# Kernel optimization log

Measured on AMD Instinct MI355X. Metric: run time of the kernel, lower is better.

The kernel has to match this reference:

```python
import jax, jax.numpy as jnp
import numpy as np

BETA = 10.0
EXTREMA = 10.0
LIK_BOUND = 1e-9
FILTERS = (1, 3, 3, 3, 3, 1)


def _sos_tanh(xf, sos_w, sos_b):
    # xf: (C,1,L). Sum-of-tanh staircase quantizer (StanH):
    # y = -extrema + sum_i 0.5*w_i*(tanh(beta*(x-b_i))+1)
    t = jnp.tanh(BETA * (xf[..., None] - sos_b))  # (C,1,L,NS)
    return -EXTREMA + jnp.sum(0.5 * sos_w * (t + 1.0), axis=-1)


def _logits_cumulative(v, mats, biases, factors):
    # v: (C,1,L); per-channel MLP with softplus-reparameterized matrices
    logits = v
    for i, m in enumerate(mats):
        logits = jnp.einsum('coi,cil->col', jax.nn.softplus(m), logits) + biases[i]
        if i < len(factors):
            logits = logits + jnp.tanh(factors[i]) * jnp.tanh(logits)
    return logits


def setup_inputs() -> dict:
    key = jax.random.key(0)
    ks = jax.random.split(key, 8)
    N, C, H, W = 8, 192, 32, 32
    NS = 60
    x = jax.random.normal(ks[0], (N, C, H, W), jnp.float32) * 3.0
    # positive step weights summing roughly to the full range
    sos_w = jax.random.uniform(ks[1], (NS,), jnp.float32, 0.1, 1.0)
    sos_w = sos_w / jnp.sum(sos_w) * (2.0 * EXTREMA)
    sos_b = jnp.linspace(-EXTREMA, EXTREMA, NS).astype(jnp.float32)
    scale = 10.0 ** (1.0 / 5.0)
    out = {'x': x, 'sos_w': sos_w, 'sos_b': sos_b}
    kk = jax.random.split(ks[2], 10)
    for i in range(5):
        init = float(np.log(np.expm1(1.0 / scale / FILTERS[i + 1])))
        out[f'm{i}'] = jnp.full((C, FILTERS[i + 1], FILTERS[i]), init, jnp.float32)
        out[f'c{i}'] = jax.random.uniform(kk[i], (C, FILTERS[i + 1], 1), jnp.float32, -0.5, 0.5)
        if i < 4:
            out[f'f{i}'] = jnp.zeros((C, FILTERS[i + 1], 1), jnp.float32)
    return out


def reference(x, sos_w, sos_b, m0, m1, m2, m3, m4, c0, c1, c2, c3, c4, f0, f1, f2, f3):
    N, C, H, W = x.shape
    mats = (m0, m1, m2, m3, m4)
    biases = (c0, c1, c2, c3, c4)
    factors = (f0, f1, f2, f3)
    # permute (N,C,H,W) -> (C,1,N*H*W) as in quantize()
    xf = jnp.transpose(x, (1, 0, 2, 3)).reshape(C, 1, -1)
    yq = _sos_tanh(xf, sos_w, sos_b)  # training-mode SoS quantization
    lower = _logits_cumulative(yq - 0.5, mats, biases, factors)
    upper = _logits_cumulative(yq + 0.5, mats, biases, factors)
    sign = jax.lax.stop_gradient(-jnp.sign(lower + upper))
    lik = jnp.abs(jax.nn.sigmoid(sign * upper) - jax.nn.sigmoid(sign * lower))
    lik = jnp.maximum(lik, LIK_BOUND)
    y_hat = jnp.transpose(yq.reshape(C, N, H, W), (1, 0, 2, 3))
    lik = jnp.transpose(lik.reshape(C, N, H, W), (1, 0, 2, 3))
    return y_hat, lik
```

## Files before the change

kernel.cpp:

```cpp
#include <hip/hip_runtime.h>
#include <math.h>

#define C_CH    192
#define HW_     1024
#define NPLANE  1536
#define TOTAL_  1572864
#define PPB     2
#define NBLK    (NPLANE / PPB)

#define LOG2E   1.4426950408889634f
#define KSOS    28.853900817779268f
#define INV_D   2.95f

#define LUT_L   512
#define LUT_X0  (-10.72f)
#define LUT_SPAN 21.44f
#define LUT_H   (LUT_SPAN / (LUT_L - 1))
#define LUT_IH  ((LUT_L - 1) / LUT_SPAN)

__device__ __forceinline__ float rcp_f(float v)  { return __builtin_amdgcn_rcpf(v); }
__device__ __forceinline__ float exp2_f(float v) { return __builtin_amdgcn_exp2f(v); }

__device__ __forceinline__ float fast_tanh(float z) {
  float e = exp2_f(z * (2.0f * LOG2E));
  return 1.0f - 2.0f * rcp_f(e + 1.0f);
}
__device__ __forceinline__ float fast_sigmoid(float z) {
  return rcp_f(1.0f + exp2_f(-z * LOG2E));
}
__device__ __forceinline__ float softplus_f(float v) {
  return log1pf(expf(v));
}

__device__ __forceinline__ float mlp_full(float v, const float* P) {
  float t, a0, a1, a2, d0, d1, d2;
  t = fmaf(P[27], v, P[33]); a0 = fmaf(P[46], fast_tanh(t), t);
  t = fmaf(P[28], v, P[34]); a1 = fmaf(P[47], fast_tanh(t), t);
  t = fmaf(P[29], v, P[35]); a2 = fmaf(P[48], fast_tanh(t), t);

  t = fmaf(P[2], a2, fmaf(P[1], a1, fmaf(P[0], a0, P[36]))); d0 = fmaf(P[49], fast_tanh(t), t);
  t = fmaf(P[5], a2, fmaf(P[4], a1, fmaf(P[3], a0, P[37]))); d1 = fmaf(P[50], fast_tanh(t), t);
  t = fmaf(P[8], a2, fmaf(P[7], a1, fmaf(P[6], a0, P[38]))); d2 = fmaf(P[51], fast_tanh(t), t);

  t = fmaf(P[11], d2, fmaf(P[10], d1, fmaf(P[9],  d0, P[39]))); a0 = fmaf(P[52], fast_tanh(t), t);
  t = fmaf(P[14], d2, fmaf(P[13], d1, fmaf(P[12], d0, P[40]))); a1 = fmaf(P[53], fast_tanh(t), t);
  t = fmaf(P[17], d2, fmaf(P[16], d1, fmaf(P[15], d0, P[41]))); a2 = fmaf(P[54], fast_tanh(t), t);

  t = fmaf(P[20], a2, fmaf(P[19], a1, fmaf(P[18], a0, P[42]))); d0 = fmaf(P[55], fast_tanh(t), t);
  t = fmaf(P[23], a2, fmaf(P[22], a1, fmaf(P[21], a0, P[43]))); d1 = fmaf(P[56], fast_tanh(t), t);
  t = fmaf(P[26], a2, fmaf(P[25], a1, fmaf(P[24], a0, P[44]))); d2 = fmaf(P[57], fast_tanh(t), t);

  return fmaf(P[32], d2, fmaf(P[31], d1, fmaf(P[30], d0, P[45])));
}

__device__ __forceinline__ float mlp_fast(float v, const float* P) {
  float a0, a1, a2, d0, d1, d2;
  a0 = fmaf(P[27], v, P[33]);
  a1 = fmaf(P[28], v, P[34]);
  a2 = fmaf(P[29], v, P[35]);

  d0 = fmaf(P[2], a2, fmaf(P[1], a1, fmaf(P[0], a0, P[36])));
  d1 = fmaf(P[5], a2, fmaf(P[4], a1, fmaf(P[3], a0, P[37])));
  d2 = fmaf(P[8], a2, fmaf(P[7], a1, fmaf(P[6], a0, P[38])));

  a0 = fmaf(P[11], d2, fmaf(P[10], d1, fmaf(P[9],  d0, P[39])));
  a1 = fmaf(P[14], d2, fmaf(P[13], d1, fmaf(P[12], d0, P[40])));
  a2 = fmaf(P[17], d2, fmaf(P[16], d1, fmaf(P[15], d0, P[41])));

  d0 = fmaf(P[20], a2, fmaf(P[19], a1, fmaf(P[18], a0, P[42])));
  d1 = fmaf(P[23], a2, fmaf(P[22], a1, fmaf(P[21], a0, P[43])));
  d2 = fmaf(P[26], a2, fmaf(P[25], a1, fmaf(P[24], a0, P[44])));

  return fmaf(P[32], d2, fmaf(P[31], d1, fmaf(P[30], d0, P[45])));
}

__device__ __forceinline__ void load_tables(
    int t, int c,
    const float* __restrict__ sos_w, const float* __restrict__ sos_b,
    const float* __restrict__ m0, const float* __restrict__ m1,
    const float* __restrict__ m2, const float* __restrict__ m3,
    const float* __restrict__ m4,
    const float* __restrict__ c0, const float* __restrict__ c1,
    const float* __restrict__ c2, const float* __restrict__ c3,
    const float* __restrict__ c4,
    const float* __restrict__ f0, const float* __restrict__ f1,
    const float* __restrict__ f2, const float* __restrict__ f3,
    float* s_w, float* s_kb, float* s_pw, float* s_p)
{
  if (t < 68) {
    float w = (t < 60) ? sos_w[t] : 0.0f;
    float b = (t < 60) ? sos_b[t] : 0.0f;
    s_w[t]  = w;
    s_kb[t] = KSOS * b;
  }
  if (t >= 64 && t < 128) {
    int i = t - 64;
    float v = (i < 60) ? sos_w[i] : 0.0f;
    float s = v;
    #pragma unroll
    for (int off = 1; off < 64; off <<= 1) {
      float o = __shfl_up(s, off, 64);
      if (i >= off) s += o;
    }
    if (i <= 60) s_pw[i] = s - v;
  }
  {
    int p = t - 128;
    if (p >= 0 && p < 58) {
      float val;
      if      (p <  9) val = softplus_f(m1[c*9 +  p      ]);
      else if (p < 18) val = softplus_f(m2[c*9 + (p -  9)]);
      else if (p < 27) val = softplus_f(m3[c*9 + (p - 18)]);
      else if (p < 30) val = softplus_f(m0[c*3 + (p - 27)]);
      else if (p < 33) val = softplus_f(m4[c*3 + (p - 30)]);
      else if (p < 36) val = c0[c*3 + (p - 33)];
      else if (p < 39) val = c1[c*3 + (p - 36)];
      else if (p < 42) val = c2[c*3 + (p - 39)];
      else if (p < 45) val = c3[c*3 + (p - 42)];
      else if (p < 46) val = c4[c];
      else if (p < 49) val = tanhf(f0[c*3 + (p - 46)]);
      else if (p < 52) val = tanhf(f1[c*3 + (p - 49)]);
      else if (p < 55) val = tanhf(f2[c*3 + (p - 52)]);
      else             val = tanhf(f3[c*3 + (p - 55)]);
      s_p[p] = val;
    }
  }
  __syncthreads();
}

__device__ __forceinline__ float sos_eval(
    float xx, const float* s_w, const float* s_kb, const float* s_pw)
{
  float kf = ceilf((xx + 9.32f) * INV_D);
  int k = (int)kf;
  k = max(0, min(60, k));
  float acc = s_pw[k];
  float kx  = KSOS * xx;
  #pragma unroll
  for (int i = 0; i < 6; ++i) {
    float z = s_kb[k + i] - kx;
    acc = fmaf(s_w[k + i], rcp_f(1.0f + exp2_f(z)), acc);
  }
  return acc - 10.0f;
}

template <bool FAST>
__device__ __forceinline__ float lik_from_y(float yq, const float* P) {
  float lo = FAST ? mlp_fast(yq - 0.5f, P) : mlp_full(yq - 0.5f, P);
  float up = FAST ? mlp_fast(yq + 0.5f, P) : mlp_full(yq + 0.5f, P);
  float lu = lo + up;
  float sg = (lu > 0.0f) ? -1.0f : ((lu < 0.0f) ? 1.0f : 0.0f);
  float lik = fabsf(fast_sigmoid(sg * up) - fast_sigmoid(sg * lo));
  return fmaxf(lik, 1e-9f);
}

__global__ __launch_bounds__(256)
void eb_fused(const float* __restrict__ x,
              const float* __restrict__ sos_w, const float* __restrict__ sos_b,
              const float* __restrict__ m0, const float* __restrict__ m1,
              const float* __restrict__ m2, const float* __restrict__ m3,
              const float* __restrict__ m4,
              const float* __restrict__ c0, const float* __restrict__ c1,
              const float* __restrict__ c2, const float* __restrict__ c3,
              const float* __restrict__ c4,
              const float* __restrict__ f0, const float* __restrict__ f1,
              const float* __restrict__ f2, const float* __restrict__ f3,
              float* __restrict__ out)
{
  __shared__ float s_w[68], s_kb[68], s_pw[64], s_p[58];
  __shared__ float s_y[LUT_L], s_l[LUT_L];

  const int t  = threadIdx.x;
  const int c  = blockIdx.x % C_CH;
  const int g  = blockIdx.x / C_CH;
  const int p0 = (2 * g)     * C_CH + c;
  const int p1 = (2 * g + 1) * C_CH + c;

  const int base0 = p0 * HW_;
  const int base1 = p1 * HW_;
  float4 xv0 = reinterpret_cast<const float4*>(x + base0)[t];
  float4 xv1 = reinterpret_cast<const float4*>(x + base1)[t];

  load_tables(t, c, sos_w, sos_b, m0, m1, m2, m3, m4,
              c0, c1, c2, c3, c4, f0, f1, f2, f3, s_w, s_kb, s_pw, s_p);

  float P[58];
  #pragma unroll
  for (int i = 0; i < 58; ++i) P[i] = s_p[i];

  bool nofac = true;
  #pragma unroll
  for (int i = 46; i < 58; ++i) nofac &= (P[i] == 0.0f);

  if (nofac) {
    #pragma unroll
    for (int r = 0; r < LUT_L / 256; ++r) {
      int idx = t + 256 * r;
      float xg = LUT_X0 + (float)idx * LUT_H;
      float yq = sos_eval(xg, s_w, s_kb, s_pw);
      s_y[idx] = yq;
      s_l[idx] = lik_from_y<true>(yq, P);
    }
  } else {
    #pragma unroll
    for (int r = 0; r < LUT_L / 256; ++r) {
      int idx = t + 256 * r;
      float xg = LUT_X0 + (float)idx * LUT_H;
      float yq = sos_eval(xg, s_w, s_kb, s_pw);
      s_y[idx] = yq;
      s_l[idx] = lik_from_y<false>(yq, P);
    }
  }
  __syncthreads();

  float4 xvs[PPB] = {xv0, xv1};
  int bases[PPB]  = {base0, base1};
  #pragma unroll
  for (int pl = 0; pl < PPB; ++pl) {
    float xs[4] = {xvs[pl].x, xvs[pl].y, xvs[pl].z, xvs[pl].w};
    float ys[4], ls[4];
    #pragma unroll
    for (int e = 0; e < 4; ++e) {
      float xx = fminf(fmaxf(xs[e], LUT_X0), LUT_X0 + LUT_SPAN);
      float u  = (xx - LUT_X0) * LUT_IH;
      int   i  = (int)u;
      i = min(i, LUT_L - 2);
      float fr = u - (float)i;
      float y0 = s_y[i], y1 = s_y[i + 1];
      float l0 = s_l[i], l1 = s_l[i + 1];
      ys[e] = fmaf(fr, y1 - y0, y0);
      ls[e] = fmaf(fr, l1 - l0, l0);
    }
    reinterpret_cast<float4*>(out + bases[pl])[t]          = make_float4(ys[0], ys[1], ys[2], ys[3]);
    reinterpret_cast<float4*>(out + TOTAL_ + bases[pl])[t] = make_float4(ls[0], ls[1], ls[2], ls[3]);
  }
}

extern "C" void kernel_launch(void* const* d_in, const int* in_sizes, int n_in,
                              void* d_out, int out_size, void* d_ws, size_t ws_size,
                              hipStream_t stream) {
  const float* x  = (const float*)d_in[0];
  const float* sw = (const float*)d_in[1];
  const float* sb = (const float*)d_in[2];
  const float *M[5], *B[5], *F[4];

  if (n_in >= 17 && in_sizes[4] == 1728) {
    for (int i = 0; i < 5; ++i) M[i] = (const float*)d_in[3 + i];
    for (int i = 0; i < 5; ++i) B[i] = (const float*)d_in[8 + i];
    for (int i = 0; i < 4; ++i) F[i] = (const float*)d_in[13 + i];
  } else {
    M[0] = (const float*)d_in[3];  B[0] = (const float*)d_in[4];  F[0] = (const float*)d_in[5];
    M[1] = (const float*)d_in[6];  B[1] = (const float*)d_in[7];  F[1] = (const float*)d_in[8];
    M[2] = (const float*)d_in[9];  B[2] = (const float*)d_in[10]; F[2] = (const float*)d_in[11];
    M[3] = (const float*)d_in[12]; B[3] = (const float*)d_in[13]; F[3] = (const float*)d_in[14];
    M[4] = (const float*)d_in[15]; B[4] = (const float*)d_in[16];
  }

  hipLaunchKernelGGL(eb_fused, dim3(NBLK), dim3(256), 0, stream,
                     x, sw, sb,
                     M[0], M[1], M[2], M[3], M[4],
                     B[0], B[1], B[2], B[3], B[4],
                     F[0], F[1], F[2], F[3],
                     (float*)d_out);
}
```

Measured before the change: 14.33 us.

## Split LUT build into stages and overlap y_hat stores with MLP table work

```diff
diff --git a/kernel.cpp b/kernel.cpp
--- a/kernel.cpp
+++ b/kernel.cpp
@@ -72,76 +72,6 @@
   d2 = fmaf(P[26], a2, fmaf(P[25], a1, fmaf(P[24], a0, P[44])));
 
   return fmaf(P[32], d2, fmaf(P[31], d1, fmaf(P[30], d0, P[45])));
-}
-
-__device__ __forceinline__ void load_tables(
-    int t, int c,
-    const float* __restrict__ sos_w, const float* __restrict__ sos_b,
-    const float* __restrict__ m0, const float* __restrict__ m1,
-    const float* __restrict__ m2, const float* __restrict__ m3,
-    const float* __restrict__ m4,
-    const float* __restrict__ c0, const float* __restrict__ c1,
-    const float* __restrict__ c2, const float* __restrict__ c3,
-    const float* __restrict__ c4,
-    const float* __restrict__ f0, const float* __restrict__ f1,
-    const float* __restrict__ f2, const float* __restrict__ f3,
-    float* s_w, float* s_kb, float* s_pw, float* s_p)
-{
-  if (t < 68) {
-    float w = (t < 60) ? sos_w[t] : 0.0f;
-    float b = (t < 60) ? sos_b[t] : 0.0f;
-    s_w[t]  = w;
-    s_kb[t] = KSOS * b;
-  }
-  if (t >= 64 && t < 128) {
-    int i = t - 64;
-    float v = (i < 60) ? sos_w[i] : 0.0f;
-    float s = v;
-    #pragma unroll
-    for (int off = 1; off < 64; off <<= 1) {
-      float o = __shfl_up(s, off, 64);
-      if (i >= off) s += o;
-    }
-    if (i <= 60) s_pw[i] = s - v;
-  }
-  {
-    int p = t - 128;
-    if (p >= 0 && p < 58) {
-      float val;
-      if      (p <  9) val = softplus_f(m1[c*9 +  p      ]);
-      else if (p < 18) val = softplus_f(m2[c*9 + (p -  9)]);
-      else if (p < 27) val = softplus_f(m3[c*9 + (p - 18)]);
-      else if (p < 30) val = softplus_f(m0[c*3 + (p - 27)]);
-      else if (p < 33) val = softplus_f(m4[c*3 + (p - 30)]);
-      else if (p < 36) val = c0[c*3 + (p - 33)];
-      else if (p < 39) val = c1[c*3 + (p - 36)];
-      else if (p < 42) val = c2[c*3 + (p - 39)];
-      else if (p < 45) val = c3[c*3 + (p - 42)];
-      else if (p < 46) val = c4[c];
-      else if (p < 49) val = tanhf(f0[c*3 + (p - 46)]);
-      else if (p < 52) val = tanhf(f1[c*3 + (p - 49)]);
-      else if (p < 55) val = tanhf(f2[c*3 + (p - 52)]);
-      else             val = tanhf(f3[c*3 + (p - 55)]);
-      s_p[p] = val;
-    }
-  }
-  __syncthreads();
-}
-
-__device__ __forceinline__ float sos_eval(
-    float xx, const float* s_w, const float* s_kb, const float* s_pw)
-{
-  float kf = ceilf((xx + 9.32f) * INV_D);
-  int k = (int)kf;
-  k = max(0, min(60, k));
-  float acc = s_pw[k];
-  float kx  = KSOS * xx;
-  #pragma unroll
-  for (int i = 0; i < 6; ++i) {
-    float z = s_kb[k + i] - kx;
-    acc = fmaf(s_w[k + i], rcp_f(1.0f + exp2_f(z)), acc);
-  }
-  return acc - 10.0f;
 }
 
 template <bool FAST>
@@ -154,18 +84,34 @@
   return fmaxf(lik, 1e-9f);
 }
 
+__device__ __forceinline__ float sos5(
+    float xx, const float* s_w, const float* s_kb, const float* s_pw)
+{
+  float kf = ceilf((xx + 9.15254237f) * INV_D);
+  int k = (int)kf;
+  k = max(0, min(60, k));
+  float acc = s_pw[k];
+  float kx  = KSOS * xx;
+  #pragma unroll
+  for (int i = 0; i < 5; ++i) {
+    float z = s_kb[k + i] - kx;
+    acc = fmaf(s_w[k + i], rcp_f(1.0f + exp2_f(z)), acc);
+  }
+  return acc - 10.0f;
+}
+
 __global__ __launch_bounds__(256)
-void eb_fused(const float* __restrict__ x,
-              const float* __restrict__ sos_w, const float* __restrict__ sos_b,
-              const float* __restrict__ m0, const float* __restrict__ m1,
-              const float* __restrict__ m2, const float* __restrict__ m3,
-              const float* __restrict__ m4,
-              const float* __restrict__ c0, const float* __restrict__ c1,
-              const float* __restrict__ c2, const float* __restrict__ c3,
-              const float* __restrict__ c4,
-              const float* __restrict__ f0, const float* __restrict__ f1,
-              const float* __restrict__ f2, const float* __restrict__ f3,
-              float* __restrict__ out)
+void eb_fused2(const float* __restrict__ x,
+               const float* __restrict__ sos_w, const float* __restrict__ sos_b,
+               const float* __restrict__ m0, const float* __restrict__ m1,
+               const float* __restrict__ m2, const float* __restrict__ m3,
+               const float* __restrict__ m4,
+               const float* __restrict__ c0, const float* __restrict__ c1,
+               const float* __restrict__ c2, const float* __restrict__ c3,
+               const float* __restrict__ c4,
+               const float* __restrict__ f0, const float* __restrict__ f1,
+               const float* __restrict__ f2, const float* __restrict__ f3,
+               float* __restrict__ out)
 {
   __shared__ float s_w[68], s_kb[68], s_pw[64], s_p[58];
   __shared__ float s_y[LUT_L], s_l[LUT_L];
@@ -173,66 +119,122 @@
   const int t  = threadIdx.x;
   const int c  = blockIdx.x % C_CH;
   const int g  = blockIdx.x / C_CH;
-  const int p0 = (2 * g)     * C_CH + c;
-  const int p1 = (2 * g + 1) * C_CH + c;
-
-  const int base0 = p0 * HW_;
-  const int base1 = p1 * HW_;
+  const int base0 = ((2 * g)     * C_CH + c) * HW_;
+  const int base1 = ((2 * g + 1) * C_CH + c) * HW_;
+
   float4 xv0 = reinterpret_cast<const float4*>(x + base0)[t];
   float4 xv1 = reinterpret_cast<const float4*>(x + base1)[t];
 
-  load_tables(t, c, sos_w, sos_b, m0, m1, m2, m3, m4,
-              c0, c1, c2, c3, c4, f0, f1, f2, f3, s_w, s_kb, s_pw, s_p);
-
-  float P[58];
-  #pragma unroll
-  for (int i = 0; i < 58; ++i) P[i] = s_p[i];
-
-  bool nofac = true;
-  #pragma unroll
-  for (int i = 46; i < 58; ++i) nofac &= (P[i] == 0.0f);
-
-  if (nofac) {
-    #pragma unroll
-    for (int r = 0; r < LUT_L / 256; ++r) {
-      int idx = t + 256 * r;
-      float xg = LUT_X0 + (float)idx * LUT_H;
-      float yq = sos_eval(xg, s_w, s_kb, s_pw);
-      s_y[idx] = yq;
-      s_l[idx] = lik_from_y<true>(yq, P);
-    }
-  } else {
-    #pragma unroll
-    for (int r = 0; r < LUT_L / 256; ++r) {
-      int idx = t + 256 * r;
-      float xg = LUT_X0 + (float)idx * LUT_H;
-      float yq = sos_eval(xg, s_w, s_kb, s_pw);
-      s_y[idx] = yq;
-      s_l[idx] = lik_from_y<false>(yq, P);
-    }
-  }
-  __syncthreads();
-
-  float4 xvs[PPB] = {xv0, xv1};
-  int bases[PPB]  = {base0, base1};
-  #pragma unroll
-  for (int pl = 0; pl < PPB; ++pl) {
-    float xs[4] = {xvs[pl].x, xvs[pl].y, xvs[pl].z, xvs[pl].w};
-    float ys[4], ls[4];
-    #pragma unroll
-    for (int e = 0; e < 4; ++e) {
-      float xx = fminf(fmaxf(xs[e], LUT_X0), LUT_X0 + LUT_SPAN);
+  const int p = t - 128;
+  const bool havep = (p >= 0 && p < 58);
+  float raw = 0.0f;
+  if (havep) {
+    if      (p <  9) raw = m1[c*9 +  p      ];
+    else if (p < 18) raw = m2[c*9 + (p -  9)];
+    else if (p < 27) raw = m3[c*9 + (p - 18)];
+    else if (p < 30) raw = m0[c*3 + (p - 27)];
+    else if (p < 33) raw = m4[c*3 + (p - 30)];
+    else if (p < 36) raw = c0[c*3 + (p - 33)];
+    else if (p < 39) raw = c1[c*3 + (p - 36)];
+    else if (p < 42) raw = c2[c*3 + (p - 39)];
+    else if (p < 45) raw = c3[c*3 + (p - 42)];
+    else if (p < 46) raw = c4[c];
+    else if (p < 49) raw = f0[c*3 + (p - 46)];
+    else if (p < 52) raw = f1[c*3 + (p - 49)];
+    else if (p < 55) raw = f2[c*3 + (p - 52)];
+    else             raw = f3[c*3 + (p - 55)];
+  }
+
+  if (t < 68) {
+    float w = (t < 60) ? sos_w[t] : 0.0f;
+    float b = (t < 60) ? sos_b[t] : 0.0f;
+    s_w[t]  = w;
+    s_kb[t] = KSOS * b;
+  }
+  if (t >= 64 && t < 128) {
+    int i = t - 64;
+    float v = (i < 60) ? sos_w[i] : 0.0f;
+    float s = v;
+    #pragma unroll
+    for (int off = 1; off < 64; off <<= 1) {
+      float o = __shfl_up(s, off, 64);
+      if (i >= off) s += o;
+    }
+    if (i <= 60) s_pw[i] = s - v;
+  }
+  __syncthreads();
+
+  #pragma unroll
+  for (int r = 0; r < LUT_L / 256; ++r) {
+    int idx = t + 256 * r;
+    float xg = LUT_X0 + (float)idx * LUT_H;
+    s_y[idx] = sos5(xg, s_w, s_kb, s_pw);
+  }
+  __syncthreads();
+
+  float xsv[8] = {xv0.x, xv0.y, xv0.z, xv0.w, xv1.x, xv1.y, xv1.z, xv1.w};
+  int   ii[8];
+  float ff[8];
+  {
+    float ys[8];
+    #pragma unroll
+    for (int e = 0; e < 8; ++e) {
+      float xx = fminf(fmaxf(xsv[e], LUT_X0), LUT_X0 + LUT_SPAN);
       float u  = (xx - LUT_X0) * LUT_IH;
       int   i  = (int)u;
       i = min(i, LUT_L - 2);
       float fr = u - (float)i;
+      ii[e] = i; ff[e] = fr;
       float y0 = s_y[i], y1 = s_y[i + 1];
+      ys[e] = fmaf(fr, y1 - y0, y0);
+    }
+    reinterpret_cast<float4*>(out + base0)[t] = make_float4(ys[0], ys[1], ys[2], ys[3]);
+    reinterpret_cast<float4*>(out + base1)[t] = make_float4(ys[4], ys[5], ys[6], ys[7]);
+  }
+
+  if (havep) {
+    float val;
+    if      (p < 33) val = softplus_f(raw);
+    else if (p < 46) val = raw;
+    else             val = tanhf(raw);
+    s_p[p] = val;
+  }
+  __syncthreads();
+
+  float P[58];
+  #pragma unroll
+  for (int i = 0; i < 58; ++i) P[i] = s_p[i];
+
+  bool nofac = true;
+  #pragma unroll
+  for (int i = 46; i < 58; ++i) nofac &= (P[i] == 0.0f);
+
+  if (nofac) {
+    #pragma unroll
+    for (int r = 0; r < LUT_L / 256; ++r) {
+      int idx = t + 256 * r;
+      s_l[idx] = lik_from_y<true>(s_y[idx], P);
+    }
+  } else {
+    #pragma unroll
+    for (int r = 0; r < LUT_L / 256; ++r) {
+      int idx = t + 256 * r;
+      s_l[idx] = lik_from_y<false>(s_y[idx], P);
+    }
+  }
+  __syncthreads();
+
+  {
+    float ls[8];
+    #pragma unroll
+    for (int e = 0; e < 8; ++e) {
+      int   i  = ii[e];
+      float fr = ff[e];
       float l0 = s_l[i], l1 = s_l[i + 1];
-      ys[e] = fmaf(fr, y1 - y0, y0);
       ls[e] = fmaf(fr, l1 - l0, l0);
     }
-    reinterpret_cast<float4*>(out + bases[pl])[t]          = make_float4(ys[0], ys[1], ys[2], ys[3]);
-    reinterpret_cast<float4*>(out + TOTAL_ + bases[pl])[t] = make_float4(ls[0], ls[1], ls[2], ls[3]);
+    reinterpret_cast<float4*>(out + TOTAL_ + base0)[t] = make_float4(ls[0], ls[1], ls[2], ls[3]);
+    reinterpret_cast<float4*>(out + TOTAL_ + base1)[t] = make_float4(ls[4], ls[5], ls[6], ls[7]);
   }
 }
 
@@ -256,7 +258,7 @@
     M[4] = (const float*)d_in[15]; B[4] = (const float*)d_in[16];
   }
 
-  hipLaunchKernelGGL(eb_fused, dim3(NBLK), dim3(256), 0, stream,
+  hipLaunchKernelGGL(eb_fused2, dim3(NBLK), dim3(256), 0, stream,
                      x, sw, sb,
                      M[0], M[1], M[2], M[3], M[4],
                      B[0], B[1], B[2], B[3], B[4],
```

Result: faster. 11.69 us (-18.4%).
